# Performance work log

Measured on AMD Instinct MI355X. Metric: run time of the kernel, lower is better.

The kernel has to match this reference:

```python
import jax, jax.numpy as jnp
import numpy as np

C = 96          # num_features
G = 3           # deform / weight groups
K = 9           # 3x3 kernel taps
OFF_CH = G * 3 * K  # 81: offset-conv output channels


def conv3x3(x, w, b=None):
    out = jax.lax.conv_general_dilated(
        x, w, window_strides=(1, 1), padding=((1, 1), (1, 1)),
        dimension_numbers=('NCHW', 'OIHW', 'NCHW'))
    if b is not None:
        out = out + b[None, :, None, None]
    return out


def offset_gen(x):
    o1, o2, m = jnp.split(x, 3, axis=1)
    return jnp.concatenate([o1, o2], axis=1), jax.nn.sigmoid(m)


def dcn(x, offset, mask, w, b):
    # Modulated deformable conv (DCNv2): offset = [y-offsets (G*K ch), x-offsets (G*K ch)]
    N, Cx, H, W = x.shape
    Cg = Cx // G
    GK = G * K
    dy = offset[:, :GK].reshape(N, G, K, H, W)
    dx = offset[:, GK:].reshape(N, G, K, H, W)
    m = mask.reshape(N, G, K, H, W)
    ky = (jnp.arange(K) // 3 - 1).astype(x.dtype)
    kx = (jnp.arange(K) % 3 - 1).astype(x.dtype)
    # sampling positions: p = p0 + kernel_offset + learned_offset (stride 1, pad 1)
    py = dy + jnp.arange(H, dtype=x.dtype)[:, None] + ky[:, None, None]   # [N,G,K,H,W]
    px = dx + jnp.arange(W, dtype=x.dtype) + kx[:, None, None]
    y0 = jnp.floor(py)
    x0 = jnp.floor(px)
    xf = x.reshape(N, G, Cg, H * W)
    gather = jax.vmap(jax.vmap(lambda xg, ig: xg[:, ig]))  # ([Cg,HW],[KHW]) -> [Cg,KHW]
    val = jnp.zeros((N, G, Cg, K, H, W), x.dtype)
    for cy, cx in ((y0, x0), (y0, x0 + 1), (y0 + 1, x0), (y0 + 1, x0 + 1)):
        wgt = (1 - jnp.abs(py - cy)) * (1 - jnp.abs(px - cx))
        valid = (cy >= 0) & (cy <= H - 1) & (cx >= 0) & (cx <= W - 1)
        iy = jnp.clip(cy, 0, H - 1).astype(jnp.int32)
        ix = jnp.clip(cx, 0, W - 1).astype(jnp.int32)
        idx = (iy * W + ix).reshape(N, G, K * H * W)
        g = gather(xf, idx).reshape(N, G, Cg, K, H, W)
        val = val + g * (wgt * valid.astype(x.dtype))[:, :, None]
    val = val * m[:, :, None]                       # modulation
    wg = w.reshape(G, Cx // G, Cg, K)               # grouped weight [G, Cout/G, Cin/G, K]
    out = jnp.einsum('ngckhw,gock->ngohw', val, wg).reshape(N, Cx, H, W)
    return out + b[None, :, None, None]


def setup_inputs() -> dict:
    key = jax.random.key(0)
    ks = jax.random.split(key, 16)
    B, H, W = 2, 128, 128
    d = {
        'X1': jax.random.normal(ks[0], (B, C, H, W), jnp.float32),
        'X2': jax.random.normal(ks[1], (B, C, H, W), jnp.float32),
        'w_bot': jax.random.normal(ks[2], (C, 2 * C, 3, 3), jnp.float32) * 0.02,
    }
    for i in range(4):
        d[f'w_off{i+1}'] = jax.random.normal(ks[3 + i], (OFF_CH, C, 3, 3), jnp.float32) * 0.02
        d[f'w_d{i+1}'] = jax.random.normal(ks[7 + i], (C, C // G, 3, 3), jnp.float32) * 0.05
        d[f'b_d{i+1}'] = jax.random.normal(ks[11 + i], (C,), jnp.float32) * 0.01
    return d


def reference(X1, X2, w_bot, w_off1, w_off2, w_off3, w_off4,
              w_d1, b_d1, w_d2, b_d2, w_d3, b_d3, w_d4, b_d4):
    B, Cx, H, W = X1.shape
    # frames: f0 = cat(X1, X1), f1 = cat(X1, X2) along channels, flattened to (B*2, 2C, H, W)
    feat = jnp.stack([jnp.concatenate([X1, X1], axis=1),
                      jnp.concatenate([X1, X2], axis=1)], axis=1)
    feat = feat.reshape(B * 2, 2 * Cx, H, W)
    feat = conv3x3(feat, w_bot)
    for w_off, w_d, b_d in ((w_off1, w_d1, b_d1), (w_off2, w_d2, b_d2),
                            (w_off3, w_d3, b_d3), (w_off4, w_d4, b_d4)):
        off, m = offset_gen(conv3x3(feat, w_off))
        feat = dcn(feat, off, m, w_d, b_d)
    return feat[1:2]


if __name__ == '__main__':
    out = reference(**setup_inputs())
    print(out.shape)
```

## Files before the change

### kernel.cpp

```cpp
#include <hip/hip_runtime.h>

#define HW 16384
#define RSB 130

typedef short short8 __attribute__((ext_vector_type(8)));
typedef float f32x4 __attribute__((ext_vector_type(4)));
typedef unsigned short ushort8v __attribute__((ext_vector_type(8)));

__device__ __forceinline__ float b2f(unsigned short u) {
    return __uint_as_float(((unsigned)u) << 16);
}
__device__ __forceinline__ unsigned short f2b(float f) {
    unsigned u = __float_as_uint(f);
    return (unsigned short)((u + 0x7fffu + ((u >> 16) & 1u)) >> 16);
}

__global__ __launch_bounds__(256) void prep_all(
    const float* __restrict__ X1, const float* __restrict__ X2,
    const float* __restrict__ w_bot,
    const float* __restrict__ wo0, const float* __restrict__ wo1,
    const float* __restrict__ wo2, const float* __restrict__ wo3,
    const float* __restrict__ wd0, const float* __restrict__ wd1,
    const float* __restrict__ wd2, const float* __restrict__ wd3,
    unsigned short* __restrict__ wBbot, unsigned short* __restrict__ wBoff,
    unsigned short* __restrict__ wdB,  unsigned short* __restrict__ in_nhwc,
    unsigned short* __restrict__ featA, unsigned short* __restrict__ featB) {
    const int N0 = 165888, N1 = N0 + 331776, N2 = N1 + 110592,
              N3 = N2 + 393216, N4 = N3 + 24768;
    for (int idx = blockIdx.x * 256 + threadIdx.x; idx < N4; idx += 131072) {
        if (idx < N0) {
            int i = idx;
            int v = i & 7, lane = (i >> 3) & 63, t = i >> 9;
            int kc = t % 6; t /= 6;
            int tap = t % 9, nt = t / 9;
            int oc = nt * 16 + (lane & 15), cin = kc * 32 + (lane >> 4) * 8 + v;
            wBbot[i] = f2b(oc < 96 ? w_bot[(oc * 192 + cin) * 9 + tap] : 0.f);
        } else if (idx < N1) {
            int j = idx - N0;
            int l = j / 82944, i = j - l * 82944;
            const float* w = l == 0 ? wo0 : l == 1 ? wo1 : l == 2 ? wo2 : wo3;
            int v = i & 7, lane = (i >> 3) & 63, t = i >> 9;
            int kc = t % 3; t /= 3;
            int tap = t % 9, nt = t / 9;
            int oc = nt * 16 + (lane & 15), cin = kc * 32 + (lane >> 4) * 8 + v;
            wBoff[j] = f2b(oc < 81 ? w[(oc * 96 + cin) * 9 + tap] : 0.f);
        } else if (idx < N2) {
            int j = idx - N1;
            int l = j / 27648, i = j - l * 27648;
            const float* w = l == 0 ? wd0 : l == 1 ? wd1 : l == 2 ? wd2 : wd3;
            int v = i & 7, lane = (i >> 3) & 63, t = i >> 9;
            int nt = t & 1; t >>= 1;
            int tap = t % 9, g = t / 9;
            int oc = nt * 16 + (lane & 15), c = (lane >> 4) * 8 + v;
            wdB[j] = f2b(w[((g * 32 + oc) * 32 + c) * 9 + tap]);
        } else if (idx < N3) {
            int j = idx - N2;
            int cb = j >> 14, p = j & (HW - 1);
            int ch = cb * 8;
            int y = p >> 7, x = p & 127;
            ushort8v o;
#pragma unroll
            for (int q = 0; q < 8; ++q) {
                int c = ch + q;
                float v = (c < 96) ? X1[c * HW + p] : X2[(c - 96) * HW + p];
                o[q] = f2b(v);
            }
            *(ushort8v*)(in_nhwc + (size_t)((y + 1) * RSB + (x + 1)) * 192 + ch) = o;
        } else {
            int j = idx - N3;
            int bp = j / 48, c8 = j - bp * 48;
            int y, x;
            if (bp < 130)      { y = 0;   x = bp; }
            else if (bp < 260) { y = 129; x = bp - 130; }
            else { int t2 = bp - 260; y = 1 + (t2 >> 1); x = (t2 & 1) ? 129 : 0; }
            size_t pix = (size_t)y * RSB + x;
            ushort8v z = {0, 0, 0, 0, 0, 0, 0, 0};
            if (c8 < 24)      *(ushort8v*)(in_nhwc + pix * 192 + c8 * 8) = z;
            else if (c8 < 36) *(ushort8v*)(featA + pix * 96 + (c8 - 24) * 8) = z;
            else              *(ushort8v*)(featB + pix * 96 + (c8 - 36) * 8) = z;
        }
    }
}

__global__ __launch_bounds__(256) void conv_bot(const unsigned short* __restrict__ in,
                                                const unsigned short* __restrict__ wB,
                                                unsigned short* __restrict__ outb) {
    const int tid = threadIdx.x;
    const int lane = tid & 63;
    const int wid = tid >> 6;
    const int msub = wid & 1, nh = wid >> 1;
    const int pbase = blockIdx.x * 32 + msub * 16;
    const int p = pbase + (lane & 15);
    const int y = p >> 7, x = p & 127;
    const int klane = lane >> 4;
    const unsigned short* arow = in + (size_t)((y + 1) * RSB + (x + 1)) * 192 + klane * 8;
    const unsigned short* wb = wB + (size_t)(nh * 3) * 9 * 6 * 512 + lane * 8;

    f32x4 a0 = {0.f, 0.f, 0.f, 0.f};
    f32x4 a1 = {0.f, 0.f, 0.f, 0.f};
    f32x4 a2 = {0.f, 0.f, 0.f, 0.f};
#pragma unroll
    for (int tap = 0; tap < 9; ++tap) {
        const unsigned short* at = arow + ((tap / 3 - 1) * RSB + (tap % 3 - 1)) * 192;
#pragma unroll
        for (int kc = 0; kc < 6; ++kc) {
            short8 a  = *(const short8*)(at + kc * 32);
            short8 b0 = *(const short8*)(wb + ((0 * 9 + tap) * 6 + kc) * 512);
            short8 b1 = *(const short8*)(wb + ((1 * 9 + tap) * 6 + kc) * 512);
            short8 b2 = *(const short8*)(wb + ((2 * 9 + tap) * 6 + kc) * 512);
            a0 = __builtin_amdgcn_mfma_f32_16x16x32_bf16(a, b0, a0, 0, 0, 0);
            a1 = __builtin_amdgcn_mfma_f32_16x16x32_bf16(a, b1, a1, 0, 0, 0);
            a2 = __builtin_amdgcn_mfma_f32_16x16x32_bf16(a, b2, a2, 0, 0, 0);
        }
    }
    const int col = lane & 15;
#pragma unroll
    for (int r = 0; r < 4; ++r) {
        int pr = pbase + klane * 4 + r;
        int yy = pr >> 7, xx = pr & 127;
        size_t base = (size_t)((yy + 1) * RSB + (xx + 1)) * 96;
        outb[base + (nh * 3 + 0) * 16 + col] = f2b(a0[r]);
        outb[base + (nh * 3 + 1) * 16 + col] = f2b(a1[r]);
        outb[base + (nh * 3 + 2) * 16 + col] = f2b(a2[r]);
    }
}

__global__ __launch_bounds__(256) void offdcn_kernel(
    const unsigned short* __restrict__ feat,
    const unsigned short* __restrict__ wBoff,
    const unsigned short* __restrict__ wdB,
    const float* __restrict__ b_d,
    void* __restrict__ outp, int last) {
    __shared__ float s_off[32][97];

    const int tid = threadIdx.x;
    const int lane = tid & 63;
    const int w = tid >> 6;
    const int col = lane & 15, klane = lane >> 4;
    const int pb = ((blockIdx.x & 7) << 6) + (blockIdx.x >> 3);
    const int P0 = pb * 32;

    {
        const int pf = w >> 1, nh = w & 1;
        const int p = P0 + pf * 16 + col;
        const int y = p >> 7, x = p & 127;
        const unsigned short* arow = feat + (size_t)((y + 1) * RSB + (x + 1)) * 96 + klane * 8;
        const unsigned short* wb = wBoff + (size_t)(nh * 3) * 9 * 3 * 512 + lane * 8;

        f32x4 a0 = {0.f, 0.f, 0.f, 0.f};
        f32x4 a1 = {0.f, 0.f, 0.f, 0.f};
        f32x4 a2 = {0.f, 0.f, 0.f, 0.f};
#pragma unroll
        for (int tap = 0; tap < 9; ++tap) {
            const unsigned short* at = arow + ((tap / 3 - 1) * RSB + (tap % 3 - 1)) * 96;
#pragma unroll
            for (int kc = 0; kc < 3; ++kc) {
                short8 a  = *(const short8*)(at + kc * 32);
                short8 b0 = *(const short8*)(wb + ((0 * 9 + tap) * 3 + kc) * 512);
                short8 b1 = *(const short8*)(wb + ((1 * 9 + tap) * 3 + kc) * 512);
                short8 b2 = *(const short8*)(wb + ((2 * 9 + tap) * 3 + kc) * 512);
                a0 = __builtin_amdgcn_mfma_f32_16x16x32_bf16(a, b0, a0, 0, 0, 0);
                a1 = __builtin_amdgcn_mfma_f32_16x16x32_bf16(a, b1, a1, 0, 0, 0);
                a2 = __builtin_amdgcn_mfma_f32_16x16x32_bf16(a, b2, a2, 0, 0, 0);
            }
        }
#pragma unroll
        for (int r = 0; r < 4; ++r) {
            int pl = pf * 16 + klane * 4 + r;
            s_off[pl][nh * 48 + 0 * 16 + col] = a0[r];
            s_off[pl][nh * 48 + 1 * 16 + col] = a1[r];
            s_off[pl][nh * 48 + 2 * 16 + col] = a2[r];
        }
    }
    __syncthreads();

    for (int sidx = w; sidx < 6; sidx += 4) {
        const int pf = sidx & 1, g = sidx >> 1;
        const int p = P0 + pf * 16 + col;
        const int y = p >> 7, x = p & 127;
        const int pl = pf * 16 + col;
        const int coct = klane * 8;

        const unsigned short* fgc = feat + g * 32 + coct;
        const unsigned short* wb = wdB + (size_t)g * 9 * 2 * 512 + lane * 8;

        int adr[9][4];
        float wgt[9][4];
#pragma unroll
        for (int k = 0; k < 9; ++k) {
            float dy = s_off[pl][g * 9 + k];
            float dx = s_off[pl][27 + g * 9 + k];
            float mr = s_off[pl][54 + g * 9 + k];
            float m = 1.f / (1.f + __expf(-mr));

            float py = dy + (float)y + (float)(k / 3 - 1);
            float px = dx + (float)x + (float)(k % 3 - 1);
            float y0f = floorf(py), x0f = floorf(px);
            float fy = py - y0f, fx = px - x0f;
            float gy = 1.f - fy, gx = 1.f - fx;

            int py0 = (int)y0f + 1, px0 = (int)x0f + 1;
            int iy0 = min(max(py0, 0), 129);
            int iy1 = min(max(py0 + 1, 0), 129);
            int ix0 = min(max(px0, 0), 129);
            int ix1 = min(max(px0 + 1, 0), 129);

            wgt[k][0] = gy * gx * m;
            wgt[k][1] = gy * fx * m;
            wgt[k][2] = fy * gx * m;
            wgt[k][3] = fy * fx * m;

            adr[k][0] = iy0 * RSB + ix0;
            adr[k][1] = iy0 * RSB + ix1;
            adr[k][2] = iy1 * RSB + ix0;
            adr[k][3] = iy1 * RSB + ix1;
        }

        f32x4 acc0 = {0.f, 0.f, 0.f, 0.f};
        f32x4 acc1 = {0.f, 0.f, 0.f, 0.f};

        ushort8v ga[4], gb[4], gc[4];
#define LDG(buf, kk) { \
        buf[0] = *(const ushort8v*)(fgc + (size_t)adr[kk][0] * 96); \
        buf[1] = *(const ushort8v*)(fgc + (size_t)adr[kk][1] * 96); \
        buf[2] = *(const ushort8v*)(fgc + (size_t)adr[kk][2] * 96); \
        buf[3] = *(const ushort8v*)(fgc + (size_t)adr[kk][3] * 96); }
#define CMP(buf, kk) { \
        short8 a; \
        _Pragma("unroll") for (int j = 0; j < 8; ++j) { \
            float val = fmaf(wgt[kk][0], b2f(buf[0][j]), \
                        fmaf(wgt[kk][1], b2f(buf[1][j]), \
                        fmaf(wgt[kk][2], b2f(buf[2][j]), \
                             wgt[kk][3] * b2f(buf[3][j])))); \
            a[j] = (short)f2b(val); } \
        short8 b0 = *(const short8*)(wb + ((kk) * 2 + 0) * 512); \
        short8 b1 = *(const short8*)(wb + ((kk) * 2 + 1) * 512); \
        acc0 = __builtin_amdgcn_mfma_f32_16x16x32_bf16(a, b0, acc0, 0, 0, 0); \
        acc1 = __builtin_amdgcn_mfma_f32_16x16x32_bf16(a, b1, acc1, 0, 0, 0); }

        LDG(ga, 0); LDG(gb, 1); LDG(gc, 2);
        CMP(ga, 0); LDG(ga, 3);
        CMP(gb, 1); LDG(gb, 4);
        CMP(gc, 2); LDG(gc, 5);
        CMP(ga, 3); LDG(ga, 6);
        CMP(gb, 4); LDG(gb, 7);
        CMP(gc, 5); LDG(gc, 8);
        CMP(ga, 6); CMP(gb, 7); CMP(gc, 8);
#undef LDG
#undef CMP

#pragma unroll
        for (int r = 0; r < 4; ++r) {
            int pr = P0 + pf * 16 + klane * 4 + r;
            int ch0 = g * 32 + col, ch1 = g * 32 + 16 + col;
            float o0 = acc0[r] + b_d[ch0];
            float o1 = acc1[r] + b_d[ch1];
            if (!last) {
                int yy = pr >> 7, xx = pr & 127;
                unsigned short* fo = (unsigned short*)outp;
                size_t base = (size_t)((yy + 1) * RSB + (xx + 1)) * 96;
                fo[base + ch0] = f2b(o0);
                fo[base + ch1] = f2b(o1);
            } else {
                float* fo = (float*)outp;
                fo[(size_t)ch0 * HW + pr] = o0;
                fo[(size_t)ch1 * HW + pr] = o1;
            }
        }
    }
}

extern "C" void kernel_launch(void* const* d_in, const int* in_sizes, int n_in,
                              void* d_out, int out_size, void* d_ws, size_t ws_size,
                              hipStream_t stream) {
    const float* X1    = (const float*)d_in[0];
    const float* X2    = (const float*)d_in[1];
    const float* w_bot = (const float*)d_in[2];
    const float* wo0 = (const float*)d_in[3],  *wo1 = (const float*)d_in[6],
               *wo2 = (const float*)d_in[9],  *wo3 = (const float*)d_in[12];
    const float* wd0 = (const float*)d_in[4],  *wd1 = (const float*)d_in[7],
               *wd2 = (const float*)d_in[10], *wd3 = (const float*)d_in[13];
    const float* bd[4] = {(const float*)d_in[5], (const float*)d_in[8],
                          (const float*)d_in[11], (const float*)d_in[14]};

    unsigned short* in_nhwc = (unsigned short*)d_ws;
    unsigned short* featA   = in_nhwc + 3244800;
    unsigned short* featB   = featA + 1622400;
    unsigned short* wBbot   = featB + 1622400;
    unsigned short* wBoff   = wBbot + 165888;
    unsigned short* wdB     = wBoff + 4 * 82944;

    prep_all<<<512, 256, 0, stream>>>(X1, X2, w_bot, wo0, wo1, wo2, wo3,
                                      wd0, wd1, wd2, wd3,
                                      wBbot, wBoff, wdB, in_nhwc, featA, featB);
    conv_bot<<<512, 256, 0, stream>>>(in_nhwc, wBbot, featA);

    unsigned short* cur = featA;
    unsigned short* nxt = featB;
    for (int it = 0; it < 4; ++it) {
        void* outp = (it == 3) ? d_out : (void*)nxt;
        offdcn_kernel<<<512, 256, 0, stream>>>(cur, wBoff + it * 82944,
                                               wdB + it * 27648, bd[it],
                                               outp, it == 3 ? 1 : 0);
        unsigned short* t = cur; cur = nxt; nxt = t;
    }
}
```

Baseline: 122.6 us.

## Halve pixel tile to 16 per block with 3 waves each owning two N-tiles

Both conv_bot and the fused offset+DCN kernel now process 16 pixels per block using 3 waves instead of 32 pixels with 4 waves. Each wave computes two 16-channel output tiles instead of three, and in the DCN stage each wave handles one deform group, which removes the uneven 6-over-4 loop. Grid size doubles to 1024 blocks. The intent is better load balance and occupancy across CUs. In exchange, each activation fetch is reused across fewer output tiles, so there is more redundant A-operand loading per output.

```diff
diff --git a/kernel.cpp b/kernel.cpp
--- a/kernel.cpp
+++ b/kernel.cpp
@@ -82,23 +82,23 @@
     }
 }
 
-__global__ __launch_bounds__(256) void conv_bot(const unsigned short* __restrict__ in,
+__global__ __launch_bounds__(192) void conv_bot(const unsigned short* __restrict__ in,
                                                 const unsigned short* __restrict__ wB,
                                                 unsigned short* __restrict__ outb) {
     const int tid = threadIdx.x;
     const int lane = tid & 63;
-    const int wid = tid >> 6;
-    const int msub = wid & 1, nh = wid >> 1;
-    const int pbase = blockIdx.x * 32 + msub * 16;
-    const int p = pbase + (lane & 15);
+    const int w = tid >> 6;
+    const int col = lane & 15, klane = lane >> 4;
+    const int pb = ((blockIdx.x & 7) << 7) + (blockIdx.x >> 3);
+    const int pbase = pb * 16;
+    const int p = pbase + col;
     const int y = p >> 7, x = p & 127;
-    const int klane = lane >> 4;
     const unsigned short* arow = in + (size_t)((y + 1) * RSB + (x + 1)) * 192 + klane * 8;
-    const unsigned short* wb = wB + (size_t)(nh * 3) * 9 * 6 * 512 + lane * 8;
+    const int nt0 = 2 * w;
+    const unsigned short* wb = wB + (size_t)nt0 * 9 * 6 * 512 + lane * 8;
 
     f32x4 a0 = {0.f, 0.f, 0.f, 0.f};
     f32x4 a1 = {0.f, 0.f, 0.f, 0.f};
-    f32x4 a2 = {0.f, 0.f, 0.f, 0.f};
 #pragma unroll
     for (int tap = 0; tap < 9; ++tap) {
         const unsigned short* at = arow + ((tap / 3 - 1) * RSB + (tap % 3 - 1)) * 192;
@@ -107,49 +107,44 @@
             short8 a  = *(const short8*)(at + kc * 32);
             short8 b0 = *(const short8*)(wb + ((0 * 9 + tap) * 6 + kc) * 512);
             short8 b1 = *(const short8*)(wb + ((1 * 9 + tap) * 6 + kc) * 512);
-            short8 b2 = *(const short8*)(wb + ((2 * 9 + tap) * 6 + kc) * 512);
             a0 = __builtin_amdgcn_mfma_f32_16x16x32_bf16(a, b0, a0, 0, 0, 0);
             a1 = __builtin_amdgcn_mfma_f32_16x16x32_bf16(a, b1, a1, 0, 0, 0);
-            a2 = __builtin_amdgcn_mfma_f32_16x16x32_bf16(a, b2, a2, 0, 0, 0);
-        }
-    }
-    const int col = lane & 15;
+        }
+    }
 #pragma unroll
     for (int r = 0; r < 4; ++r) {
         int pr = pbase + klane * 4 + r;
         int yy = pr >> 7, xx = pr & 127;
         size_t base = (size_t)((yy + 1) * RSB + (xx + 1)) * 96;
-        outb[base + (nh * 3 + 0) * 16 + col] = f2b(a0[r]);
-        outb[base + (nh * 3 + 1) * 16 + col] = f2b(a1[r]);
-        outb[base + (nh * 3 + 2) * 16 + col] = f2b(a2[r]);
-    }
-}
-
-__global__ __launch_bounds__(256) void offdcn_kernel(
+        outb[base + (nt0 + 0) * 16 + col] = f2b(a0[r]);
+        outb[base + (nt0 + 1) * 16 + col] = f2b(a1[r]);
+    }
+}
+
+__global__ __launch_bounds__(192) void offdcn_kernel(
     const unsigned short* __restrict__ feat,
     const unsigned short* __restrict__ wBoff,
     const unsigned short* __restrict__ wdB,
     const float* __restrict__ b_d,
     void* __restrict__ outp, int last) {
-    __shared__ float s_off[32][97];
+    __shared__ float s_off[16][97];
 
     const int tid = threadIdx.x;
     const int lane = tid & 63;
     const int w = tid >> 6;
     const int col = lane & 15, klane = lane >> 4;
-    const int pb = ((blockIdx.x & 7) << 6) + (blockIdx.x >> 3);
-    const int P0 = pb * 32;
+    const int pb = ((blockIdx.x & 7) << 7) + (blockIdx.x >> 3);
+    const int P0 = pb * 16;
+    const int p = P0 + col;
+    const int y = p >> 7, x = p & 127;
 
     {
-        const int pf = w >> 1, nh = w & 1;
-        const int p = P0 + pf * 16 + col;
-        const int y = p >> 7, x = p & 127;
         const unsigned short* arow = feat + (size_t)((y + 1) * RSB + (x + 1)) * 96 + klane * 8;
-        const unsigned short* wb = wBoff + (size_t)(nh * 3) * 9 * 3 * 512 + lane * 8;
+        const int nt0 = 2 * w;
+        const unsigned short* wb = wBoff + (size_t)nt0 * 9 * 3 * 512 + lane * 8;
 
         f32x4 a0 = {0.f, 0.f, 0.f, 0.f};
         f32x4 a1 = {0.f, 0.f, 0.f, 0.f};
-        f32x4 a2 = {0.f, 0.f, 0.f, 0.f};
 #pragma unroll
         for (int tap = 0; tap < 9; ++tap) {
             const unsigned short* at = arow + ((tap / 3 - 1) * RSB + (tap % 3 - 1)) * 96;
@@ -158,27 +153,21 @@
                 short8 a  = *(const short8*)(at + kc * 32);
                 short8 b0 = *(const short8*)(wb + ((0 * 9 + tap) * 3 + kc) * 512);
                 short8 b1 = *(const short8*)(wb + ((1 * 9 + tap) * 3 + kc) * 512);
-                short8 b2 = *(const short8*)(wb + ((2 * 9 + tap) * 3 + kc) * 512);
                 a0 = __builtin_amdgcn_mfma_f32_16x16x32_bf16(a, b0, a0, 0, 0, 0);
                 a1 = __builtin_amdgcn_mfma_f32_16x16x32_bf16(a, b1, a1, 0, 0, 0);
-                a2 = __builtin_amdgcn_mfma_f32_16x16x32_bf16(a, b2, a2, 0, 0, 0);
             }
         }
 #pragma unroll
         for (int r = 0; r < 4; ++r) {
-            int pl = pf * 16 + klane * 4 + r;
-            s_off[pl][nh * 48 + 0 * 16 + col] = a0[r];
-            s_off[pl][nh * 48 + 1 * 16 + col] = a1[r];
-            s_off[pl][nh * 48 + 2 * 16 + col] = a2[r];
+            int pl = klane * 4 + r;
+            s_off[pl][(nt0 + 0) * 16 + col] = a0[r];
+            s_off[pl][(nt0 + 1) * 16 + col] = a1[r];
         }
     }
     __syncthreads();
 
-    for (int sidx = w; sidx < 6; sidx += 4) {
-        const int pf = sidx & 1, g = sidx >> 1;
-        const int p = P0 + pf * 16 + col;
-        const int y = p >> 7, x = p & 127;
-        const int pl = pf * 16 + col;
+    {
+        const int g = w;
         const int coct = klane * 8;
 
         const unsigned short* fgc = feat + g * 32 + coct;
@@ -188,9 +177,9 @@
         float wgt[9][4];
 #pragma unroll
         for (int k = 0; k < 9; ++k) {
-            float dy = s_off[pl][g * 9 + k];
-            float dx = s_off[pl][27 + g * 9 + k];
-            float mr = s_off[pl][54 + g * 9 + k];
+            float dy = s_off[col][g * 9 + k];
+            float dx = s_off[col][27 + g * 9 + k];
+            float mr = s_off[col][54 + g * 9 + k];
             float m = 1.f / (1.f + __expf(-mr));
 
             float py = dy + (float)y + (float)(k / 3 - 1);
@@ -251,7 +240,7 @@
 
 #pragma unroll
         for (int r = 0; r < 4; ++r) {
-            int pr = P0 + pf * 16 + klane * 4 + r;
+            int pr = P0 + klane * 4 + r;
             int ch0 = g * 32 + col, ch1 = g * 32 + 16 + col;
             float o0 = acc0[r] + b_d[ch0];
             float o1 = acc1[r] + b_d[ch1];
@@ -293,15 +282,15 @@
     prep_all<<<512, 256, 0, stream>>>(X1, X2, w_bot, wo0, wo1, wo2, wo3,
                                       wd0, wd1, wd2, wd3,
                                       wBbot, wBoff, wdB, in_nhwc, featA, featB);
-    conv_bot<<<512, 256, 0, stream>>>(in_nhwc, wBbot, featA);
+    conv_bot<<<1024, 192, 0, stream>>>(in_nhwc, wBbot, featA);
 
     unsigned short* cur = featA;
     unsigned short* nxt = featB;
     for (int it = 0; it < 4; ++it) {
         void* outp = (it == 3) ? d_out : (void*)nxt;
-        offdcn_kernel<<<512, 256, 0, stream>>>(cur, wBoff + it * 82944,
-                                               wdB + it * 27648, bd[it],
-                                               outp, it == 3 ? 1 : 0);
+        offdcn_kernel<<<1024, 192, 0, stream>>>(cur, wBoff + it * 82944,
+                                                wdB + it * 27648, bd[it],
+                                                outp, it == 3 ? 1 : 0);
         unsigned short* t = cur; cur = nxt; nxt = t;
     }
 }
```

Measured after the change: 127.2 us. +3.7%, slower.

## Stage conv_bot weights in LDS with double-buffered async global-to-LDS loads

Applied to the files above, without the earlier changes.

conv_bot now copies each tap's weight slice into shared memory using global_load_lds, double-buffered so the next tap's weights load while the current tap's MFMAs run. All four waves in a block then read B fragments from LDS instead of each fetching them from global memory. Blocks are also remapped with the same interleaved pixel-block order used in offdcn_kernel. The per-tap __syncthreads and the rolled tap loop add barrier and loop overhead, and 72 KB of LDS per block may limit occupancy.

```diff
diff --git a/kernel.cpp b/kernel.cpp
--- a/kernel.cpp
+++ b/kernel.cpp
@@ -6,6 +6,11 @@
 typedef short short8 __attribute__((ext_vector_type(8)));
 typedef float f32x4 __attribute__((ext_vector_type(4)));
 typedef unsigned short ushort8v __attribute__((ext_vector_type(8)));
+
+typedef __attribute__((address_space(1))) const unsigned int* gas_ptr;
+typedef __attribute__((address_space(3))) unsigned int* las_ptr;
+#define GLOAD_LDS16(g, l) \
+    __builtin_amdgcn_global_load_lds((gas_ptr)(const void*)(g), (las_ptr)(void*)(l), 16, 0, 0)
 
 __device__ __forceinline__ float b2f(unsigned short u) {
     return __uint_as_float(((unsigned)u) << 16);
@@ -85,43 +90,69 @@
 __global__ __launch_bounds__(256) void conv_bot(const unsigned short* __restrict__ in,
                                                 const unsigned short* __restrict__ wB,
                                                 unsigned short* __restrict__ outb) {
+    __shared__ unsigned short s_b[2][18432];
+
     const int tid = threadIdx.x;
     const int lane = tid & 63;
     const int wid = tid >> 6;
     const int msub = wid & 1, nh = wid >> 1;
-    const int pbase = blockIdx.x * 32 + msub * 16;
+    const int pb = ((blockIdx.x & 7) << 6) + (blockIdx.x >> 3);
+    const int pbase = pb * 32 + msub * 16;
     const int p = pbase + (lane & 15);
     const int y = p >> 7, x = p & 127;
     const int klane = lane >> 4;
     const unsigned short* arow = in + (size_t)((y + 1) * RSB + (x + 1)) * 192 + klane * 8;
-    const unsigned short* wb = wB + (size_t)(nh * 3) * 9 * 6 * 512 + lane * 8;
+    const int nt0 = nh * 3;
+    const int col = lane & 15;
+
+#pragma unroll
+    for (int i = 0; i < 9; ++i) {
+        int c = wid * 9 + i;
+        int nt = c / 6, kc = c - nt * 6;
+        const unsigned short* g = wB + ((size_t)(nt * 9 + 0) * 6 + kc) * 512 + lane * 8;
+        GLOAD_LDS16(g, &s_b[0][c * 512]);
+    }
+    __syncthreads();
 
     f32x4 a0 = {0.f, 0.f, 0.f, 0.f};
     f32x4 a1 = {0.f, 0.f, 0.f, 0.f};
     f32x4 a2 = {0.f, 0.f, 0.f, 0.f};
-#pragma unroll
+
+#pragma unroll 1
     for (int tap = 0; tap < 9; ++tap) {
-        const unsigned short* at = arow + ((tap / 3 - 1) * RSB + (tap % 3 - 1)) * 192;
+        const int cur = tap & 1;
+        if (tap < 8) {
+            const int nxt = cur ^ 1;
+#pragma unroll
+            for (int i = 0; i < 9; ++i) {
+                int c = wid * 9 + i;
+                int nt = c / 6, kc = c - nt * 6;
+                const unsigned short* g = wB + ((size_t)(nt * 9 + tap + 1) * 6 + kc) * 512 + lane * 8;
+                GLOAD_LDS16(g, &s_b[nxt][c * 512]);
+            }
+        }
+        const int toff = ((tap / 3 - 1) * RSB + (tap % 3 - 1)) * 192;
 #pragma unroll
         for (int kc = 0; kc < 6; ++kc) {
-            short8 a  = *(const short8*)(at + kc * 32);
-            short8 b0 = *(const short8*)(wb + ((0 * 9 + tap) * 6 + kc) * 512);
-            short8 b1 = *(const short8*)(wb + ((1 * 9 + tap) * 6 + kc) * 512);
-            short8 b2 = *(const short8*)(wb + ((2 * 9 + tap) * 6 + kc) * 512);
+            short8 a  = *(const short8*)(arow + toff + kc * 32);
+            short8 b0 = *(const short8*)(&s_b[cur][((nt0 + 0) * 6 + kc) * 512 + lane * 8]);
+            short8 b1 = *(const short8*)(&s_b[cur][((nt0 + 1) * 6 + kc) * 512 + lane * 8]);
+            short8 b2 = *(const short8*)(&s_b[cur][((nt0 + 2) * 6 + kc) * 512 + lane * 8]);
             a0 = __builtin_amdgcn_mfma_f32_16x16x32_bf16(a, b0, a0, 0, 0, 0);
             a1 = __builtin_amdgcn_mfma_f32_16x16x32_bf16(a, b1, a1, 0, 0, 0);
             a2 = __builtin_amdgcn_mfma_f32_16x16x32_bf16(a, b2, a2, 0, 0, 0);
         }
-    }
-    const int col = lane & 15;
+        __syncthreads();
+    }
+
 #pragma unroll
     for (int r = 0; r < 4; ++r) {
         int pr = pbase + klane * 4 + r;
         int yy = pr >> 7, xx = pr & 127;
         size_t base = (size_t)((yy + 1) * RSB + (xx + 1)) * 96;
-        outb[base + (nh * 3 + 0) * 16 + col] = f2b(a0[r]);
-        outb[base + (nh * 3 + 1) * 16 + col] = f2b(a1[r]);
-        outb[base + (nh * 3 + 2) * 16 + col] = f2b(a2[r]);
+        outb[base + (nt0 + 0) * 16 + col] = f2b(a0[r]);
+        outb[base + (nt0 + 1) * 16 + col] = f2b(a1[r]);
+        outb[base + (nt0 + 2) * 16 + col] = f2b(a2[r]);
     }
 }
 
```

After: 120.0 us. -2.1%, faster.
